# Kernel tuning notes

Measured on AMD Instinct MI355X. Metric: run time of the kernel, lower is better.

The kernel has to match this reference:

```python
import jax, jax.numpy as jnp
import numpy as np

HID = 64


def setup_inputs() -> dict:
    key = jax.random.key(0)
    k = jax.random.split(key, 7)
    B, T = 4096, 8192
    x = jax.random.normal(k[0], (B, T, 1), dtype=jnp.float32)
    # Kaiming-uniform-ish init scale; exact values irrelevant for correctness baseline
    W_in = jax.random.normal(k[1], (1, HID), dtype=jnp.float32) * 0.5
    b_in = jax.random.normal(k[2], (HID,), dtype=jnp.float32) * 0.1
    W_s = jax.random.normal(k[3], (HID, HID), dtype=jnp.float32) * (1.0 / np.sqrt(HID))
    b_s = jax.random.normal(k[4], (HID,), dtype=jnp.float32) * 0.1
    W_out = jax.random.normal(k[5], (HID, 1), dtype=jnp.float32) * (1.0 / np.sqrt(HID))
    b_out = jax.random.normal(k[6], (1,), dtype=jnp.float32) * 0.1
    return {"x": x, "W_in": W_in, "b_in": b_in, "W_s": W_s, "b_s": b_s,
            "W_out": W_out, "b_out": b_out}


def reference(x, W_in, b_in, W_s, b_s, W_out, b_out):
    B, T, _ = x.shape
    xt = jnp.swapaxes(x, 0, 1)  # [T, B, 1] -> scan over time

    def step(h, x_t):
        # input_proj on [B,1] -> [B,HID]; tiny GEMM per step (the recurrence is sequential)
        inp = x_t @ W_in + b_in
        h = jax.nn.gelu(h @ W_s + b_s + inp, approximate=False)  # torch GELU = exact erf
        return h, None

    h0 = jnp.zeros((B, HID), dtype=x.dtype)
    h_final, _ = jax.lax.scan(step, h0, xt)
    return h_final @ W_out + b_out  # [B, 1]
```

## Files before the change

kernel.cpp:

```cpp
#include <hip/hip_runtime.h>
#include <cstdint>
#include <cstddef>

#define HID 64
#define RPG 16
#define HSTR 72

typedef short bf16x8 __attribute__((ext_vector_type(8)));
typedef float f32x4 __attribute__((ext_vector_type(4)));
typedef float f32x2 __attribute__((ext_vector_type(2)));

__device__ __forceinline__ float fast_gelu(float z) {
    float u = z * 0.70710678118654752f;
    float a = __builtin_fabsf(u);
    float t = __builtin_amdgcn_rcpf(__builtin_fmaf(0.3275911f, a, 1.0f));
    float e = __builtin_amdgcn_exp2f((u * u) * -1.44269504088896f);
    float p =                   1.061405429f;
    p = __builtin_fmaf(p, t, -1.453152027f);
    p = __builtin_fmaf(p, t,  1.421413741f);
    p = __builtin_fmaf(p, t, -0.284496736f);
    p = __builtin_fmaf(p, t,  0.254829592f);
    p = p * t;
    float er = __builtin_fmaf(-p, e, 1.0f);
    er = __builtin_copysignf(er, u);
    float zh = 0.5f * z;
    return __builtin_fmaf(zh, er, zh);
}

__device__ __forceinline__ ushort bf16_hi(float f) {
    return (ushort)(__float_as_uint(f) >> 16);
}
__device__ __forceinline__ float bf16_f(ushort u) {
    return __uint_as_float(((unsigned)u) << 16);
}

#define STEP(RHI, RLO, WHI, WLO, E0, E1) { \
    const bf16x8 Ahi0 = *reinterpret_cast<const bf16x8*>(RHI); \
    const bf16x8 Ahi1 = *reinterpret_cast<const bf16x8*>((RHI) + 32); \
    const bf16x8 Alo0 = *reinterpret_cast<const bf16x8*>(RLO); \
    const bf16x8 Alo1 = *reinterpret_cast<const bf16x8*>((RLO) + 32); \
    const f32x2 xr = *reinterpret_cast<const f32x2*>(&xlds[tl][4 * q + E0]); \
    const f32x4 zz = {0.f, 0.f, 0.f, 0.f}; \
    f32x4 ahh = __builtin_amdgcn_mfma_f32_16x16x32_bf16(Ahi0, Bhi0, zz, 0, 0, 0); \
    f32x4 ac1 = __builtin_amdgcn_mfma_f32_16x16x32_bf16(Ahi0, Blo0, zz, 0, 0, 0); \
    f32x4 ac2 = __builtin_amdgcn_mfma_f32_16x16x32_bf16(Alo0, Bhi0, zz, 0, 0, 0); \
    ahh = __builtin_amdgcn_mfma_f32_16x16x32_bf16(Ahi1, Bhi1, ahh, 0, 0, 0); \
    ac1 = __builtin_amdgcn_mfma_f32_16x16x32_bf16(Ahi1, Blo1, ac1, 0, 0, 0); \
    ac2 = __builtin_amdgcn_mfma_f32_16x16x32_bf16(Alo1, Bhi1, ac2, 0, 0, 0); \
    const float z0 = (ahh[E0] + ac1[E0]) + (ac2[E0] + __builtin_fmaf(xr[0], win, cb)); \
    const float z1 = (ahh[E1] + ac1[E1]) + (ac2[E1] + __builtin_fmaf(xr[1], win, cb)); \
    const float h0 = fast_gelu(z0); \
    const float h1 = fast_gelu(z1); \
    const unsigned hb0 = __float_as_uint(h0), hb1 = __float_as_uint(h1); \
    (WHI)[0]    = (ushort)(hb0 >> 16); \
    (WHI)[HSTR] = (ushort)(hb1 >> 16); \
    (WLO)[0]    = bf16_hi(h0 - __uint_as_float(hb0 & 0xffff0000u)); \
    (WLO)[HSTR] = bf16_hi(h1 - __uint_as_float(hb1 & 0xffff0000u)); \
    __syncthreads(); }

#define MAINLOOP(E0, E1) { \
    ushort* const whi1 = &hlds[1][0][(4 * q + E0) * HSTR + c]; \
    ushort* const wlo1 = &hlds[1][1][(4 * q + E0) * HSTR + c]; \
    ushort* const whi0 = &hlds[0][0][(4 * q + E0) * HSTR + c]; \
    ushort* const wlo0 = &hlds[0][1][(4 * q + E0) * HSTR + c]; \
    for (int tc = 0; tc < nch; ++tc) { \
        xlds[lane][ww]     = x[(size_t)(bA + ww) * (size_t)T + (size_t)(tc * 64) + lane]; \
        xlds[lane][ww + 8] = x[(size_t)(bA + ww + 8) * (size_t)T + (size_t)(tc * 64) + lane]; \
        __syncthreads(); \
        _Pragma("unroll 1") \
        for (int tl2 = 0; tl2 < 32; ++tl2) { \
            { const int tl = 2 * tl2;     STEP(rhi0, rlo0, whi1, wlo1, E0, E1) } \
            { const int tl = 2 * tl2 + 1; STEP(rhi1, rlo1, whi0, wlo0, E0, E1) } \
        } \
    } }

__global__ __launch_bounds__(512, 2)
void ssm_kernel(const float* __restrict__ x,
                const float* __restrict__ W_in,
                const float* __restrict__ b_in,
                const float* __restrict__ W_s,
                const float* __restrict__ b_s,
                const float* __restrict__ W_out,
                const float* __restrict__ b_out,
                float* __restrict__ out,
                int B, int T) {
    __shared__ ushort hlds[2][2][RPG * HSTR];
    __shared__ float  xlds[64][RPG];

    const int tid  = threadIdx.x;
    const int ww   = tid >> 6;
    const int g    = ww & 3;
    const int hf   = ww >> 2;
    const int lane = tid & 63;
    const int q    = lane >> 4;
    const int rr   = lane & 15;
    const int bA   = blockIdx.x * RPG;
    const int c    = (g << 4) | rr;

    if (bA >= B) return;

    bf16x8 Bhi0, Bhi1, Blo0, Blo1;
#pragma unroll
    for (int e = 0; e < 8; ++e) {
        {
            const float wf = W_s[(q * 8 + e) * HID + c];
            const ushort hi = bf16_hi(wf);
            Bhi0[e] = (short)hi;
            Blo0[e] = (short)bf16_hi(wf - bf16_f(hi));
        }
        {
            const float wf = W_s[(32 + q * 8 + e) * HID + c];
            const ushort hi = bf16_hi(wf);
            Bhi1[e] = (short)hi;
            Blo1[e] = (short)bf16_hi(wf - bf16_f(hi));
        }
    }
    asm volatile("" : "+v"(Bhi0), "+v"(Bhi1), "+v"(Blo0), "+v"(Blo1));

    const float win = W_in[c];
    const float cb  = b_in[c] + b_s[c];

    {
        ushort* p = &hlds[0][0][0];
        for (int i = tid; i < 2 * RPG * HSTR; i += 512) p[i] = 0;
    }

    const ushort* const rhi0 = &hlds[0][0][rr * HSTR + q * 8];
    const ushort* const rlo0 = &hlds[0][1][rr * HSTR + q * 8];
    const ushort* const rhi1 = &hlds[1][0][rr * HSTR + q * 8];
    const ushort* const rlo1 = &hlds[1][1][rr * HSTR + q * 8];

    const int nch = T >> 6;

    if (hf == 0) { MAINLOOP(0, 1) } else { MAINLOOP(2, 3) }

    if (hf == 0) {
        const int row = (g << 2) + q;
        const int c4  = rr << 2;
        const ushort* hp = &hlds[0][0][row * HSTR + c4];
        const ushort* lp = &hlds[0][1][row * HSTR + c4];
        float s = 0.f;
#pragma unroll
        for (int j = 0; j < 4; ++j) {
            const float hv = bf16_f(hp[j]) + bf16_f(lp[j]);
            s = __builtin_fmaf(hv, W_out[c4 + j], s);
        }
        s += __shfl_xor(s, 1, 64);
        s += __shfl_xor(s, 2, 64);
        s += __shfl_xor(s, 4, 64);
        s += __shfl_xor(s, 8, 64);
        if (rr == 0) out[bA + row] = s + b_out[0];
    }
}

extern "C" void kernel_launch(void* const* d_in, const int* in_sizes, int n_in,
                              void* d_out, int out_size, void* d_ws, size_t ws_size,
                              hipStream_t stream) {
    const float* x     = (const float*)d_in[0];
    const float* W_in  = (const float*)d_in[1];
    const float* b_in  = (const float*)d_in[2];
    const float* W_s   = (const float*)d_in[3];
    const float* b_s   = (const float*)d_in[4];
    const float* W_out = (const float*)d_in[5];
    const float* b_out = (const float*)d_in[6];
    float* out = (float*)d_out;

    const int B = out_size;
    const int T = in_sizes[0] / B;

    const int blocks = B / RPG;
    ssm_kernel<<<blocks, 512, 0, stream>>>(
        x, W_in, b_in, W_s, b_s, W_out, b_out, out, B, T);
}
```

Before: 2.817 ms.

## Transpose recurrent MFMA so each lane owns one batch row with packed writes

Swaps the MFMA operand roles: W_s becomes the A operand and the hidden state the B operand, so each lane's outputs are two adjacent hidden columns of a single batch row. This allows packed 32-bit LDS writes of the hi/lo bf16 pairs instead of four 16-bit stores. It also lets one vectorized x load per four timesteps replace a per-step x read, using a padded row-major x tile. The final output projection is reworked to use a single wave, with 16 columns per lane and a shorter shuffle reduction.

After: 2.641 ms. 1.07x faster.

```diff
diff --git a/kernel.cpp b/kernel.cpp
--- a/kernel.cpp
+++ b/kernel.cpp
@@ -5,10 +5,10 @@
 #define HID 64
 #define RPG 16
 #define HSTR 72
+#define XSTR 68
 
 typedef short bf16x8 __attribute__((ext_vector_type(8)));
 typedef float f32x4 __attribute__((ext_vector_type(4)));
-typedef float f32x2 __attribute__((ext_vector_type(2)));
 
 __device__ __forceinline__ float fast_gelu(float z) {
     float u = z * 0.70710678118654752f;
@@ -34,43 +34,54 @@
     return __uint_as_float(((unsigned)u) << 16);
 }
 
-#define STEP(RHI, RLO, WHI, WLO, E0, E1) { \
-    const bf16x8 Ahi0 = *reinterpret_cast<const bf16x8*>(RHI); \
-    const bf16x8 Ahi1 = *reinterpret_cast<const bf16x8*>((RHI) + 32); \
-    const bf16x8 Alo0 = *reinterpret_cast<const bf16x8*>(RLO); \
-    const bf16x8 Alo1 = *reinterpret_cast<const bf16x8*>((RLO) + 32); \
-    const f32x2 xr = *reinterpret_cast<const f32x2*>(&xlds[tl][4 * q + E0]); \
+#define STEP(RHI, RLO, WHI, WLO, XB, E0, E1) { \
+    const bf16x8 Hhi0 = *reinterpret_cast<const bf16x8*>(RHI); \
+    const bf16x8 Hhi1 = *reinterpret_cast<const bf16x8*>((RHI) + 32); \
+    const bf16x8 Hlo0 = *reinterpret_cast<const bf16x8*>(RLO); \
+    const bf16x8 Hlo1 = *reinterpret_cast<const bf16x8*>((RLO) + 32); \
     const f32x4 zz = {0.f, 0.f, 0.f, 0.f}; \
-    f32x4 ahh = __builtin_amdgcn_mfma_f32_16x16x32_bf16(Ahi0, Bhi0, zz, 0, 0, 0); \
-    f32x4 ac1 = __builtin_amdgcn_mfma_f32_16x16x32_bf16(Ahi0, Blo0, zz, 0, 0, 0); \
-    f32x4 ac2 = __builtin_amdgcn_mfma_f32_16x16x32_bf16(Alo0, Bhi0, zz, 0, 0, 0); \
-    ahh = __builtin_amdgcn_mfma_f32_16x16x32_bf16(Ahi1, Bhi1, ahh, 0, 0, 0); \
-    ac1 = __builtin_amdgcn_mfma_f32_16x16x32_bf16(Ahi1, Blo1, ac1, 0, 0, 0); \
-    ac2 = __builtin_amdgcn_mfma_f32_16x16x32_bf16(Alo1, Bhi1, ac2, 0, 0, 0); \
-    const float z0 = (ahh[E0] + ac1[E0]) + (ac2[E0] + __builtin_fmaf(xr[0], win, cb)); \
-    const float z1 = (ahh[E1] + ac1[E1]) + (ac2[E1] + __builtin_fmaf(xr[1], win, cb)); \
+    f32x4 ahh = __builtin_amdgcn_mfma_f32_16x16x32_bf16(Whi0, Hhi0, zz, 0, 0, 0); \
+    f32x4 ac1 = __builtin_amdgcn_mfma_f32_16x16x32_bf16(Whi0, Hlo0, zz, 0, 0, 0); \
+    f32x4 ac2 = __builtin_amdgcn_mfma_f32_16x16x32_bf16(Wlo0, Hhi0, zz, 0, 0, 0); \
+    ahh = __builtin_amdgcn_mfma_f32_16x16x32_bf16(Whi1, Hhi1, ahh, 0, 0, 0); \
+    ac1 = __builtin_amdgcn_mfma_f32_16x16x32_bf16(Whi1, Hlo1, ac1, 0, 0, 0); \
+    ac2 = __builtin_amdgcn_mfma_f32_16x16x32_bf16(Wlo1, Hhi1, ac2, 0, 0, 0); \
+    const float z0 = (ahh[E0] + ac1[E0]) + (ac2[E0] + __builtin_fmaf((XB), win0, cb0)); \
+    const float z1 = (ahh[E1] + ac1[E1]) + (ac2[E1] + __builtin_fmaf((XB), win1, cb1)); \
     const float h0 = fast_gelu(z0); \
     const float h1 = fast_gelu(z1); \
     const unsigned hb0 = __float_as_uint(h0), hb1 = __float_as_uint(h1); \
-    (WHI)[0]    = (ushort)(hb0 >> 16); \
-    (WHI)[HSTR] = (ushort)(hb1 >> 16); \
-    (WLO)[0]    = bf16_hi(h0 - __uint_as_float(hb0 & 0xffff0000u)); \
-    (WLO)[HSTR] = bf16_hi(h1 - __uint_as_float(hb1 & 0xffff0000u)); \
+    *(WHI) = (hb0 >> 16) | (hb1 & 0xffff0000u); \
+    const float l0 = h0 - __uint_as_float(hb0 & 0xffff0000u); \
+    const float l1 = h1 - __uint_as_float(hb1 & 0xffff0000u); \
+    *(WLO) = (__float_as_uint(l0) >> 16) | (__float_as_uint(l1) & 0xffff0000u); \
     __syncthreads(); }
 
 #define MAINLOOP(E0, E1) { \
-    ushort* const whi1 = &hlds[1][0][(4 * q + E0) * HSTR + c]; \
-    ushort* const wlo1 = &hlds[1][1][(4 * q + E0) * HSTR + c]; \
-    ushort* const whi0 = &hlds[0][0][(4 * q + E0) * HSTR + c]; \
-    ushort* const wlo0 = &hlds[0][1][(4 * q + E0) * HSTR + c]; \
+    const float win0 = W_in[cq + E0]; \
+    const float win1 = W_in[cq + E1]; \
+    const float cb0  = b_in[cq + E0] + b_s[cq + E0]; \
+    const float cb1  = b_in[cq + E1] + b_s[cq + E1]; \
+    const ushort* const rhiA = &hlds[0][0][rr * HSTR + 8 * q]; \
+    const ushort* const rloA = &hlds[0][1][rr * HSTR + 8 * q]; \
+    const ushort* const rhiB = &hlds[1][0][rr * HSTR + 8 * q]; \
+    const ushort* const rloB = &hlds[1][1][rr * HSTR + 8 * q]; \
+    unsigned* const whiA = reinterpret_cast<unsigned*>(&hlds[0][0][rr * HSTR + cq + E0]); \
+    unsigned* const wloA = reinterpret_cast<unsigned*>(&hlds[0][1][rr * HSTR + cq + E0]); \
+    unsigned* const whiB = reinterpret_cast<unsigned*>(&hlds[1][0][rr * HSTR + cq + E0]); \
+    unsigned* const wloB = reinterpret_cast<unsigned*>(&hlds[1][1][rr * HSTR + cq + E0]); \
     for (int tc = 0; tc < nch; ++tc) { \
-        xlds[lane][ww]     = x[(size_t)(bA + ww) * (size_t)T + (size_t)(tc * 64) + lane]; \
-        xlds[lane][ww + 8] = x[(size_t)(bA + ww + 8) * (size_t)T + (size_t)(tc * 64) + lane]; \
+        const size_t tg = (size_t)tc * 64; \
+        xlds[ww][lane]     = x[(size_t)(bA + ww) * (size_t)T + tg + lane]; \
+        xlds[ww + 8][lane] = x[(size_t)(bA + ww + 8) * (size_t)T + tg + lane]; \
         __syncthreads(); \
         _Pragma("unroll 1") \
-        for (int tl2 = 0; tl2 < 32; ++tl2) { \
-            { const int tl = 2 * tl2;     STEP(rhi0, rlo0, whi1, wlo1, E0, E1) } \
-            { const int tl = 2 * tl2 + 1; STEP(rhi1, rlo1, whi0, wlo0, E0, E1) } \
+        for (int t4 = 0; t4 < 16; ++t4) { \
+            const f32x4 xq = *reinterpret_cast<const f32x4*>(&xlds[rr][t4 * 4]); \
+            STEP(rhiA, rloA, whiB, wloB, xq[0], E0, E1) \
+            STEP(rhiB, rloB, whiA, wloA, xq[1], E0, E1) \
+            STEP(rhiA, rloA, whiB, wloB, xq[2], E0, E1) \
+            STEP(rhiB, rloB, whiA, wloA, xq[3], E0, E1) \
         } \
     } }
 
@@ -85,7 +96,7 @@
                 float* __restrict__ out,
                 int B, int T) {
     __shared__ ushort hlds[2][2][RPG * HSTR];
-    __shared__ float  xlds[64][RPG];
+    __shared__ float  xlds[RPG][XSTR];
 
     const int tid  = threadIdx.x;
     const int ww   = tid >> 6;
@@ -95,61 +106,44 @@
     const int q    = lane >> 4;
     const int rr   = lane & 15;
     const int bA   = blockIdx.x * RPG;
-    const int c    = (g << 4) | rr;
+    const int cq   = 16 * g + 4 * q;
 
-    if (bA >= B) return;
-
-    bf16x8 Bhi0, Bhi1, Blo0, Blo1;
+    bf16x8 Whi0, Whi1, Wlo0, Wlo1;
+    const int wcol = 16 * g + rr;
 #pragma unroll
     for (int e = 0; e < 8; ++e) {
-        {
-            const float wf = W_s[(q * 8 + e) * HID + c];
+        {   const float wf = W_s[(8 * q + e) * HID + wcol];
             const ushort hi = bf16_hi(wf);
-            Bhi0[e] = (short)hi;
-            Blo0[e] = (short)bf16_hi(wf - bf16_f(hi));
-        }
-        {
-            const float wf = W_s[(32 + q * 8 + e) * HID + c];
+            Whi0[e] = (short)hi;
+            Wlo0[e] = (short)bf16_hi(wf - bf16_f(hi)); }
+        {   const float wf = W_s[(32 + 8 * q + e) * HID + wcol];
             const ushort hi = bf16_hi(wf);
-            Bhi1[e] = (short)hi;
-            Blo1[e] = (short)bf16_hi(wf - bf16_f(hi));
-        }
+            Whi1[e] = (short)hi;
+            Wlo1[e] = (short)bf16_hi(wf - bf16_f(hi)); }
     }
-    asm volatile("" : "+v"(Bhi0), "+v"(Bhi1), "+v"(Blo0), "+v"(Blo1));
-
-    const float win = W_in[c];
-    const float cb  = b_in[c] + b_s[c];
+    asm volatile("" : "+v"(Whi0), "+v"(Whi1), "+v"(Wlo0), "+v"(Wlo1));
 
     {
         ushort* p = &hlds[0][0][0];
         for (int i = tid; i < 2 * RPG * HSTR; i += 512) p[i] = 0;
     }
 
-    const ushort* const rhi0 = &hlds[0][0][rr * HSTR + q * 8];
-    const ushort* const rlo0 = &hlds[0][1][rr * HSTR + q * 8];
-    const ushort* const rhi1 = &hlds[1][0][rr * HSTR + q * 8];
-    const ushort* const rlo1 = &hlds[1][1][rr * HSTR + q * 8];
-
     const int nch = T >> 6;
 
     if (hf == 0) { MAINLOOP(0, 1) } else { MAINLOOP(2, 3) }
 
-    if (hf == 0) {
-        const int row = (g << 2) + q;
-        const int c4  = rr << 2;
-        const ushort* hp = &hlds[0][0][row * HSTR + c4];
-        const ushort* lp = &hlds[0][1][row * HSTR + c4];
+    if (ww == 0) {
+        const int r  = lane >> 2;
+        const int p4 = lane & 3;
+        const ushort* hp = &hlds[0][0][r * HSTR + p4 * 16];
+        const ushort* lp = &hlds[0][1][r * HSTR + p4 * 16];
         float s = 0.f;
 #pragma unroll
-        for (int j = 0; j < 4; ++j) {
-            const float hv = bf16_f(hp[j]) + bf16_f(lp[j]);
-            s = __builtin_fmaf(hv, W_out[c4 + j], s);
-        }
+        for (int j = 0; j < 16; ++j)
+            s = __builtin_fmaf(bf16_f(hp[j]) + bf16_f(lp[j]), W_out[p4 * 16 + j], s);
         s += __shfl_xor(s, 1, 64);
         s += __shfl_xor(s, 2, 64);
-        s += __shfl_xor(s, 4, 64);
-        s += __shfl_xor(s, 8, 64);
-        if (rr == 0) out[bA + row] = s + b_out[0];
+        if (p4 == 0) out[bA + r] = s + b_out[0];
     }
 }
 
```
